# Kernel tuning notes

Hardware: AMD Instinct MI355X
Metric: run time of the kernel (lower is better)

The kernel has to match this reference:

```python
import jax, jax.numpy as jnp
import numpy as np

STARTS = (0, 752, 184, 568)  # 4 fixed 16-wide channel regions inside 768
EMBED = 16


def setup_inputs() -> dict:
    key = jax.random.key(0)
    k = jax.random.split(key, 5)
    B = 131072
    r = 8
    return {
        "base": jax.random.normal(k[0], (1, B, 768), dtype=jnp.float32),
        "Wp": jax.random.normal(k[1], (4, r, EMBED), dtype=jnp.float32) * (1.0 / np.sqrt(EMBED)),
        "bp": jax.random.normal(k[2], (4, r), dtype=jnp.float32) * 0.02,
        "Ws": jax.random.normal(k[3], (4, r, EMBED), dtype=jnp.float32) * (1.0 / np.sqrt(EMBED)),
        "bs": jax.random.normal(k[4], (4, r), dtype=jnp.float32) * 0.02,
    }


def reference(base, Wp, bp, Ws, bs):
    # base: [1, B, 768]; Wp/Ws: [4, r, 16]; bp/bs: [4, r]
    # NoReFT per region: h + Wp^T((Ws h + bs) - (Wp h + bp)); act_fn is 'linear'.
    x = jnp.stack([base[0, :, s:s + EMBED] for s in STARTS])  # [4, B, 16]
    proj = jnp.einsum('gbe,gre->gbr', x, Wp) + bp[:, None, :]  # [4, B, r]
    src = jnp.einsum('gbe,gre->gbr', x, Ws) + bs[:, None, :]   # [4, B, r]
    delta = jnp.einsum('gbr,gre->gbe', src - proj, Wp)         # [4, B, 16]
    out = base
    for i, s in enumerate(STARTS):
        out = out.at[0, :, s:s + EMBED].add(delta[i])
    return out
```

## Files before the change

kernel.cpp:

```cpp
#include <hip/hip_runtime.h>


constexpr int ROWS_PER_BLOCK = 8;
constexpr int F4_PER_ROW = 192;

__global__ __launch_bounds__(192) void multi_mini_interv_kernel(
    const float* __restrict__ base,
    const float* __restrict__ Wp,
    const float* __restrict__ bp,
    const float* __restrict__ Ws,
    const float* __restrict__ bs,
    float* __restrict__ out,
    int B)
{
    __shared__ float sWp[512];
    __shared__ float sWd[512];
    __shared__ float sbd[32];

    const int tid = threadIdx.x;

    for (int i = tid; i < 512; i += 192) {
        float wp = Wp[i];
        sWp[i] = wp;
        sWd[i] = Ws[i] - wp;
    }
    if (tid < 32) sbd[tid] = bs[tid] - bp[tid];
    __syncthreads();

    const int c = tid;
    int g = -1, cbase = 0;
    if (c < 4)                    { g = 0; cbase = 0;   }
    else if (c >= 188)            { g = 1; cbase = 188; }
    else if (c >= 46 && c < 50)   { g = 2; cbase = 46;  }
    else if (c >= 142 && c < 146) { g = 3; cbase = 142; }
    const int off = (c - cbase) * 4;

    const float4* __restrict__ base4 = (const float4*)base;
    float4* __restrict__ out4 = (float4*)out;

    const int row0 = blockIdx.x * ROWS_PER_BLOCK;
    #pragma unroll
    for (int rr = 0; rr < ROWS_PER_BLOCK; ++rr) {
        const int row = row0 + rr;
        if (row >= B) break;
        const float4* __restrict__ src = base4 + (size_t)row * F4_PER_ROW;
        float4 v = src[c];

        if (g >= 0) {
            float x[16];
            float4 x0 = src[cbase + 0];
            float4 x1 = src[cbase + 1];
            float4 x2 = src[cbase + 2];
            float4 x3 = src[cbase + 3];
            x[0]  = x0.x; x[1]  = x0.y; x[2]  = x0.z; x[3]  = x0.w;
            x[4]  = x1.x; x[5]  = x1.y; x[6]  = x1.z; x[7]  = x1.w;
            x[8]  = x2.x; x[9]  = x2.y; x[10] = x2.z; x[11] = x2.w;
            x[12] = x3.x; x[13] = x3.y; x[14] = x3.z; x[15] = x3.w;

            float t[8];
            const float* wd = &sWd[g * 128];
            #pragma unroll
            for (int r = 0; r < 8; ++r) {
                float acc = sbd[g * 8 + r];
                #pragma unroll
                for (int e = 0; e < 16; ++e)
                    acc += x[e] * wd[r * 16 + e];
                t[r] = acc;
            }

            float d0 = 0.f, d1 = 0.f, d2 = 0.f, d3 = 0.f;
            const float* wp = &sWp[g * 128 + off];
            #pragma unroll
            for (int r = 0; r < 8; ++r) {
                const float tr = t[r];
                d0 += tr * wp[r * 16 + 0];
                d1 += tr * wp[r * 16 + 1];
                d2 += tr * wp[r * 16 + 2];
                d3 += tr * wp[r * 16 + 3];
            }
            v.x += d0; v.y += d1; v.z += d2; v.w += d3;
        }

        out4[(size_t)row * F4_PER_ROW + c] = v;
    }
}

extern "C" void kernel_launch(void* const* d_in, const int* in_sizes, int n_in,
                              void* d_out, int out_size, void* d_ws, size_t ws_size,
                              hipStream_t stream) {
    const float* base = (const float*)d_in[0];
    const float* Wp   = (const float*)d_in[1];
    const float* bp   = (const float*)d_in[2];
    const float* Ws   = (const float*)d_in[3];
    const float* bs   = (const float*)d_in[4];
    float* out = (float*)d_out;

    const int B = in_sizes[0] / 768;
    const int grid = (B + ROWS_PER_BLOCK - 1) / ROWS_PER_BLOCK;

    multi_mini_interv_kernel<<<grid, 192, 0, stream>>>(base, Wp, bp, Ws, bs, out, B);
}
```

Measured before the change: 652.2 us.

## Fold low-rank projection into per-thread 16x4 matrix with persistent grid-stride loop

```diff
diff --git a/kernel.cpp b/kernel.cpp
--- a/kernel.cpp
+++ b/kernel.cpp
@@ -1,10 +1,14 @@
 #include <hip/hip_runtime.h>
 
 
-constexpr int ROWS_PER_BLOCK = 8;
-constexpr int F4_PER_ROW = 192;
+typedef float f4 __attribute__((ext_vector_type(4)));
 
-__global__ __launch_bounds__(192) void multi_mini_interv_kernel(
+constexpr int F4_PER_ROW   = 192;
+constexpr int ROWS_PER_ITER = 4;
+constexpr int BLOCK = 192;
+constexpr int MAX_BLOCKS = 2048;
+
+__global__ __launch_bounds__(BLOCK) void multi_mini_interv_kernel(
     const float* __restrict__ base,
     const float* __restrict__ Wp,
     const float* __restrict__ bp,
@@ -19,7 +23,7 @@
 
     const int tid = threadIdx.x;
 
-    for (int i = tid; i < 512; i += 192) {
+    for (int i = tid; i < 512; i += BLOCK) {
         float wp = Wp[i];
         sWp[i] = wp;
         sWd[i] = Ws[i] - wp;
@@ -35,53 +39,99 @@
     else if (c >= 142 && c < 146) { g = 3; cbase = 142; }
     const int off = (c - cbase) * 4;
 
-    const float4* __restrict__ base4 = (const float4*)base;
-    float4* __restrict__ out4 = (float4*)out;
+    float M[16][4];
+    float dv[4] = {0.f, 0.f, 0.f, 0.f};
+    if (g >= 0) {
+        #pragma unroll
+        for (int e = 0; e < 16; ++e) {
+            M[e][0] = 0.f; M[e][1] = 0.f; M[e][2] = 0.f; M[e][3] = 0.f;
+        }
+        const float* wd = &sWd[g * 128];
+        const float* wp = &sWp[g * 128 + off];
+        #pragma unroll
+        for (int r = 0; r < 8; ++r) {
+            const float w0 = wp[r * 16 + 0];
+            const float w1 = wp[r * 16 + 1];
+            const float w2 = wp[r * 16 + 2];
+            const float w3 = wp[r * 16 + 3];
+            const float bd = sbd[g * 8 + r];
+            dv[0] += bd * w0; dv[1] += bd * w1; dv[2] += bd * w2; dv[3] += bd * w3;
+            #pragma unroll
+            for (int e = 0; e < 16; ++e) {
+                const float wde = wd[r * 16 + e];
+                M[e][0] += wde * w0; M[e][1] += wde * w1;
+                M[e][2] += wde * w2; M[e][3] += wde * w3;
+            }
+        }
+    }
 
-    const int row0 = blockIdx.x * ROWS_PER_BLOCK;
-    #pragma unroll
-    for (int rr = 0; rr < ROWS_PER_BLOCK; ++rr) {
-        const int row = row0 + rr;
-        if (row >= B) break;
-        const float4* __restrict__ src = base4 + (size_t)row * F4_PER_ROW;
-        float4 v = src[c];
+    const f4* __restrict__ base4 = (const f4*)base;
+    f4* __restrict__ out4 = (f4*)out;
+
+    const int ngroups_full = B / ROWS_PER_ITER;
+
+    for (int grp = blockIdx.x; grp < ngroups_full; grp += gridDim.x) {
+        const size_t row0 = (size_t)grp * ROWS_PER_ITER;
+        const f4* __restrict__ src = base4 + row0 * F4_PER_ROW;
+        f4* __restrict__ dst = out4 + row0 * F4_PER_ROW;
+
+        f4 v[ROWS_PER_ITER];
+        #pragma unroll
+        for (int rr = 0; rr < ROWS_PER_ITER; ++rr)
+            v[rr] = src[rr * F4_PER_ROW + c];
 
         if (g >= 0) {
-            float x[16];
-            float4 x0 = src[cbase + 0];
-            float4 x1 = src[cbase + 1];
-            float4 x2 = src[cbase + 2];
-            float4 x3 = src[cbase + 3];
-            x[0]  = x0.x; x[1]  = x0.y; x[2]  = x0.z; x[3]  = x0.w;
-            x[4]  = x1.x; x[5]  = x1.y; x[6]  = x1.z; x[7]  = x1.w;
-            x[8]  = x2.x; x[9]  = x2.y; x[10] = x2.z; x[11] = x2.w;
-            x[12] = x3.x; x[13] = x3.y; x[14] = x3.z; x[15] = x3.w;
-
-            float t[8];
-            const float* wd = &sWd[g * 128];
             #pragma unroll
-            for (int r = 0; r < 8; ++r) {
-                float acc = sbd[g * 8 + r];
+            for (int rr = 0; rr < ROWS_PER_ITER; ++rr) {
+                const f4* s = src + rr * F4_PER_ROW + cbase;
+                f4 x0 = s[0], x1 = s[1], x2 = s[2], x3 = s[3];
+                float x[16];
                 #pragma unroll
-                for (int e = 0; e < 16; ++e)
-                    acc += x[e] * wd[r * 16 + e];
-                t[r] = acc;
+                for (int q = 0; q < 4; ++q) {
+                    x[q]      = x0[q];
+                    x[4 + q]  = x1[q];
+                    x[8 + q]  = x2[q];
+                    x[12 + q] = x3[q];
+                }
+                float d0 = dv[0], d1 = dv[1], d2 = dv[2], d3 = dv[3];
+                #pragma unroll
+                for (int e = 0; e < 16; ++e) {
+                    d0 += x[e] * M[e][0];
+                    d1 += x[e] * M[e][1];
+                    d2 += x[e] * M[e][2];
+                    d3 += x[e] * M[e][3];
+                }
+                v[rr][0] += d0; v[rr][1] += d1; v[rr][2] += d2; v[rr][3] += d3;
             }
-
-            float d0 = 0.f, d1 = 0.f, d2 = 0.f, d3 = 0.f;
-            const float* wp = &sWp[g * 128 + off];
-            #pragma unroll
-            for (int r = 0; r < 8; ++r) {
-                const float tr = t[r];
-                d0 += tr * wp[r * 16 + 0];
-                d1 += tr * wp[r * 16 + 1];
-                d2 += tr * wp[r * 16 + 2];
-                d3 += tr * wp[r * 16 + 3];
-            }
-            v.x += d0; v.y += d1; v.z += d2; v.w += d3;
         }
 
-        out4[(size_t)row * F4_PER_ROW + c] = v;
+        #pragma unroll
+        for (int rr = 0; rr < ROWS_PER_ITER; ++rr)
+            __builtin_nontemporal_store(v[rr], &dst[rr * F4_PER_ROW + c]);
+    }
+
+    const int tail0 = ngroups_full * ROWS_PER_ITER;
+    for (int row = tail0 + blockIdx.x; row < B; row += gridDim.x) {
+        const f4* __restrict__ s = base4 + (size_t)row * F4_PER_ROW;
+        f4 v = s[c];
+        if (g >= 0) {
+            f4 x0 = s[cbase + 0], x1 = s[cbase + 1], x2 = s[cbase + 2], x3 = s[cbase + 3];
+            float x[16];
+            #pragma unroll
+            for (int q = 0; q < 4; ++q) {
+                x[q] = x0[q]; x[4 + q] = x1[q]; x[8 + q] = x2[q]; x[12 + q] = x3[q];
+            }
+            float d0 = dv[0], d1 = dv[1], d2 = dv[2], d3 = dv[3];
+            #pragma unroll
+            for (int e = 0; e < 16; ++e) {
+                d0 += x[e] * M[e][0];
+                d1 += x[e] * M[e][1];
+                d2 += x[e] * M[e][2];
+                d3 += x[e] * M[e][3];
+            }
+            v[0] += d0; v[1] += d1; v[2] += d2; v[3] += d3;
+        }
+        __builtin_nontemporal_store(v, out4 + (size_t)row * F4_PER_ROW + c);
     }
 }
 
@@ -96,7 +146,8 @@
     float* out = (float*)d_out;
 
     const int B = in_sizes[0] / 768;
-    const int grid = (B + ROWS_PER_BLOCK - 1) / ROWS_PER_BLOCK;
+    int ngroups = (B + ROWS_PER_ITER - 1) / ROWS_PER_ITER;
+    int grid = ngroups < MAX_BLOCKS ? ngroups : MAX_BLOCKS;
 
-    multi_mini_interv_kernel<<<grid, 192, 0, stream>>>(base, Wp, bp, Ws, bs, out, B);
+    multi_mini_interv_kernel<<<grid, BLOCK, 0, stream>>>(base, Wp, bp, Ws, bs, out, B);
 }
```

Result: no change. 653.3 us (+0.2%).
